# Optimization experiments

Measured on AMD Instinct MI355X. Metric: run time of the kernel, lower is better.

The kernel has to match this reference:

```python
import jax, jax.numpy as jnp
import numpy as np

NUM_HEADS = 32


def setup_inputs() -> dict:
    key = jax.random.key(0)
    ks = jax.random.split(key, 6)
    B, S, D = 1, 2048, 4096
    hd = D // NUM_HEADS  # 128
    x = jax.random.normal(ks[0], (B, S, D), dtype=jnp.float32)
    # true rotary frequencies: freqs_cis = exp(i * t * theta^{-2j/hd})
    inv_freq = 1.0 / (10000.0 ** (jnp.arange(0, hd, 2, dtype=jnp.float32) / hd))  # [hd//2]
    angles = jnp.arange(S, dtype=jnp.float32)[:, None] * inv_freq[None, :]  # [S, hd//2]
    freqs_cos = jnp.cos(angles)
    freqs_sin = jnp.sin(angles)
    scale = 0.02
    wq = jax.random.normal(ks[1], (D, D), dtype=jnp.float32) * scale
    wk = jax.random.normal(ks[2], (D, D), dtype=jnp.float32) * scale
    wv = jax.random.normal(ks[3], (D, D), dtype=jnp.float32) * scale
    wo = jax.random.normal(ks[4], (D, D), dtype=jnp.float32) * scale
    return {"x": x, "freqs_cos": freqs_cos, "freqs_sin": freqs_sin,
            "wq": wq, "wk": wk, "wv": wv, "wo": wo}


def _apply_rope(t, cos, sin):
    # t: [B, S, H, hd]; cos/sin: [S, hd//2]
    B, S, H, hd = t.shape
    tr = t.reshape(B, S, H, hd // 2, 2)
    a, b = tr[..., 0], tr[..., 1]
    c = cos[None, :, None, :]
    s = sin[None, :, None, :]
    out_r = a * c - b * s
    out_i = a * s + b * c
    return jnp.stack([out_r, out_i], axis=-1).reshape(B, S, H, hd)


def reference(x, freqs_cos, freqs_sin, wq, wk, wv, wo):
    B, S, D = x.shape
    H = NUM_HEADS
    hd = D // H
    xq = (x @ wq).reshape(B, S, H, hd)
    xk = (x @ wk).reshape(B, S, H, hd)
    xv = (x @ wv).reshape(B, S, H, hd)
    xq = _apply_rope(xq, freqs_cos, freqs_sin)
    xk = _apply_rope(xk, freqs_cos, freqs_sin)
    # [B, H, S, hd]
    xq = xq.transpose(0, 2, 1, 3)
    xk = xk.transpose(0, 2, 1, 3)
    xv = xv.transpose(0, 2, 1, 3)
    scores = jnp.einsum('bhqd,bhkd->bhqk', xq, xk) / jnp.sqrt(jnp.float32(hd))
    scores = jax.nn.softmax(scores.astype(jnp.float32), axis=-1).astype(xq.dtype)
    out = jnp.einsum('bhqk,bhkd->bhqd', scores, xv)
    out = out.transpose(0, 2, 1, 3).reshape(B, S, D)
    return out @ wo
```

## Files before the change

### kernel.cpp

```cpp
#include <hip/hip_runtime.h>
#include <hip/hip_bf16.h>

typedef __hip_bfloat16 bf16;
typedef __attribute__((ext_vector_type(8))) short short8;
typedef __attribute__((ext_vector_type(4))) short short4v;
typedef __attribute__((ext_vector_type(4))) float f32x4;

#define MFMA16(a, b, c) __builtin_amdgcn_mfma_f32_16x16x32_bf16((a), (b), (c), 0, 0, 0)

static __device__ __forceinline__ void gload_lds16(const bf16* g, bf16* l) {
  __builtin_amdgcn_global_load_lds((const __attribute__((address_space(1))) unsigned int*)g,
                                   (__attribute__((address_space(3))) unsigned int*)l,
                                   16, 0, 0);
}

__global__ __launch_bounds__(256) void castx_kernel(const float* __restrict__ x,
                                                    bf16* __restrict__ xb, int n) {
  int i = (blockIdx.x * 256 + threadIdx.x) * 8;
  if (i >= n) return;
  float4 v0 = *(const float4*)(x + i);
  float4 v1 = *(const float4*)(x + i + 4);
  bf16 tmp[8];
  tmp[0] = __float2bfloat16(v0.x); tmp[1] = __float2bfloat16(v0.y);
  tmp[2] = __float2bfloat16(v0.z); tmp[3] = __float2bfloat16(v0.w);
  tmp[4] = __float2bfloat16(v1.x); tmp[5] = __float2bfloat16(v1.y);
  tmp[6] = __float2bfloat16(v1.z); tmp[7] = __float2bfloat16(v1.w);
  *(short8*)(xb + i) = *(short8*)tmp;
}

__global__ __launch_bounds__(256) void tw_kernel(const float* __restrict__ W,
                                                 bf16* __restrict__ WT) {
  __shared__ bf16 tile[64][65];
  int b = blockIdx.x;
  int tk = (b >> 6) * 64;
  int tn = (b & 63) * 64;
  int t = threadIdx.x;
  int c = t & 63, r0 = t >> 6;
#pragma unroll
  for (int i = 0; i < 16; ++i) {
    int r = i * 4 + r0;
    tile[c][r] = __float2bfloat16(W[(size_t)(tk + r) * 4096 + tn + c]);
  }
  __syncthreads();
#pragma unroll
  for (int i = 0; i < 16; ++i) {
    int r = i * 4 + r0;
    WT[(size_t)(tn + r) * 4096 + tk + c] = tile[r][c];
  }
}

template <int EPI>
__global__ __launch_bounds__(512) void gemm_bt2(const bf16* __restrict__ A,
                                                const bf16* __restrict__ Bt,
                                                void* __restrict__ Cv,
                                                int M, int N, int K,
                                                const float* __restrict__ fcos,
                                                const float* __restrict__ fsin) {
  __shared__ bf16 LDS[3][384 * 64];
  const int NB = N >> 8;
  int bm = blockIdx.x / NB, bn = blockIdx.x % NB;
  int t = threadIdx.x, lane = t & 63, w = t >> 6;
  int wm = w >> 2, wn = w & 3;
  int lr = lane & 15, lg = lane >> 4;
  f32x4 acc[4][4] = {};

  const bf16* Ab = A + (size_t)bm * 128 * K;
  const bf16* Bb = Bt + (size_t)bn * 256 * K;
  int srow = t >> 3;
  int sg = (t & 7) ^ (((t >> 5) & 1) << 1);
  int NK = K >> 6;

#define GSTAGE(buf, kt)                                                         \
  do {                                                                          \
    bf16* l_ = LDS[buf];                                                        \
    const bf16* ga_ = Ab + (size_t)(kt) * 64;                                   \
    _Pragma("unroll") for (int i = 0; i < 2; ++i)                               \
      gload_lds16(ga_ + (size_t)(i * 64 + srow) * K + sg * 8,                   \
                  l_ + (i * 512 + w * 64) * 8);                                 \
    const bf16* gb_ = Bb + (size_t)(kt) * 64;                                   \
    bf16* lb_ = l_ + 128 * 64;                                                  \
    _Pragma("unroll") for (int i = 0; i < 4; ++i)                               \
      gload_lds16(gb_ + (size_t)(i * 64 + srow) * K + sg * 8,                   \
                  lb_ + (i * 512 + w * 64) * 8);                                \
  } while (0)

  GSTAGE(0, 0);
  GSTAGE(1, 1);
  asm volatile("s_waitcnt vmcnt(6)" ::: "memory");
  __builtin_amdgcn_s_barrier();

  int cr = 0;
  for (int kt = 0; kt < NK; ++kt) {
    const bf16* la = LDS[cr];
    const bf16* lb = la + 128 * 64;
    int sw = (lr >> 1) & 2;

    short8 a[4][2], b0[2][2];
#pragma unroll
    for (int m = 0; m < 4; ++m)
#pragma unroll
      for (int kc = 0; kc < 2; ++kc)
        a[m][kc] = *(const short8*)(la + (wm * 64 + m * 16 + lr) * 64 +
                                    (((kc * 4 + lg) ^ sw) << 3));
#pragma unroll
    for (int n2 = 0; n2 < 2; ++n2)
#pragma unroll
      for (int kc = 0; kc < 2; ++kc)
        b0[n2][kc] = *(const short8*)(lb + (wn * 64 + n2 * 16 + lr) * 64 +
                                      (((kc * 4 + lg) ^ sw) << 3));
    int cw = cr + 2; if (cw >= 3) cw -= 3;
    if (kt + 2 < NK) {
      GSTAGE(cw, kt + 2);
      asm volatile("s_waitcnt vmcnt(6)" ::: "memory");
    } else {
      asm volatile("s_waitcnt vmcnt(0)" ::: "memory");
    }
    __builtin_amdgcn_s_barrier();
    __builtin_amdgcn_s_setprio(1);
#pragma unroll
    for (int m = 0; m < 4; ++m)
#pragma unroll
      for (int n2 = 0; n2 < 2; ++n2)
#pragma unroll
        for (int kc = 0; kc < 2; ++kc)
          acc[m][n2] = MFMA16(a[m][kc], b0[n2][kc], acc[m][n2]);
    __builtin_amdgcn_s_setprio(0);
    __builtin_amdgcn_s_barrier();

    short8 b1[2][2];
#pragma unroll
    for (int n2 = 0; n2 < 2; ++n2)
#pragma unroll
      for (int kc = 0; kc < 2; ++kc)
        b1[n2][kc] = *(const short8*)(lb + (wn * 64 + (2 + n2) * 16 + lr) * 64 +
                                      (((kc * 4 + lg) ^ sw) << 3));
    __builtin_amdgcn_s_barrier();
    __builtin_amdgcn_s_setprio(1);
#pragma unroll
    for (int m = 0; m < 4; ++m)
#pragma unroll
      for (int n2 = 0; n2 < 2; ++n2)
#pragma unroll
        for (int kc = 0; kc < 2; ++kc)
          acc[m][2 + n2] = MFMA16(a[m][kc], b1[n2][kc], acc[m][2 + n2]);
    __builtin_amdgcn_s_setprio(0);
    __builtin_amdgcn_s_barrier();

    cr = (cr + 1 == 3) ? 0 : cr + 1;
  }
#undef GSTAGE

#pragma unroll
  for (int m = 0; m < 4; ++m)
#pragma unroll
    for (int nf = 0; nf < 4; ++nf) {
      int col = bn * 256 + wn * 64 + nf * 16 + lr;
      int row0 = bm * 128 + wm * 64 + m * 16 + lg * 4;
      if constexpr (EPI == 1 || EPI == 2) {
        const float qs = (EPI == 1) ? 0.08838834764831845f : 1.0f;
        int ip = (col >> 1) & 63;
        float sgn = (col & 1) ? 1.0f : -1.0f;
#pragma unroll
        for (int r = 0; r < 4; ++r) {
          int row = row0 + r;
          float mine = acc[m][nf][r];
          float oth = __shfl_xor(mine, 1);
          float cv = fcos[row * 64 + ip];
          float sv = fsin[row * 64 + ip];
          float v = (mine * cv + sgn * oth * sv) * qs;
          ((bf16*)Cv)[(size_t)row * N + col] = __float2bfloat16(v);
        }
      } else if constexpr (EPI == 3) {
        bf16 tmp[4];
#pragma unroll
        for (int r = 0; r < 4; ++r) tmp[r] = __float2bfloat16(acc[m][nf][r]);
        *(short4v*)((bf16*)Cv + (size_t)col * M + row0) = *(short4v*)tmp;
      } else {
#pragma unroll
        for (int r = 0; r < 4; ++r) {
          int row = row0 + r;
          if constexpr (EPI == 4)
            ((float*)Cv)[(size_t)row * N + col] = acc[m][nf][r];
          else
            ((bf16*)Cv)[(size_t)row * N + col] = __float2bfloat16(acc[m][nf][r]);
        }
      }
    }
}

__global__ __launch_bounds__(512, 2) void attn_fwd(const bf16* __restrict__ Q,
                                                   const bf16* __restrict__ K,
                                                   const bf16* __restrict__ Vt,
                                                   bf16* __restrict__ O) {
  __shared__ bf16 Kbuf[2][64 * 128];
  __shared__ bf16 Vbuf[2][128 * 64];
  __shared__ char Ps_all[8][2][2048];
  const int S = 2048, D = 4096, HD = 128, NT = 32;
  int g = blockIdx.y * 8 + blockIdx.x;
  int wid = (g & 7) * 32 + (g >> 3);
  int h = wid >> 3, qb = wid & 7;
  int tid = threadIdx.x, lane = tid & 63, w = tid >> 6;
  int lr = lane & 15, lg = lane >> 4;
  int q0 = qb * 256 + w * 32;
  int swz = (lr & 7) << 4;

  const bf16* Kh = K + h * HD;
  const bf16* Vh = Vt + (size_t)h * HD * S;

  short8 aq[2][4];
#pragma unroll
  for (int u = 0; u < 2; ++u)
#pragma unroll
    for (int c = 0; c < 4; ++c)
      aq[u][c] = *(const short8*)(Q + (size_t)(q0 + u * 16 + lr) * D + h * HD + c * 32 + lg * 8);

  int kr = lane >> 4, ksl = lane & 15;
  int vr = lane >> 3, vsl = lane & 7;

  f32x4 accO[2][8] = {};
  float lsum[2] = {0.f, 0.f};

#define STAGE(b, ttile)                                                            \
  do {                                                                             \
    int kv0_ = (ttile) * 64;                                                       \
    _Pragma("unroll") for (int ii = 0; ii < 2; ++ii) {                             \
      int row = w * 8 + ii * 4 + kr;                                               \
      gload_lds16(Kh + (size_t)(kv0_ + row) * D + ((ksl ^ (row & 7)) << 3),        \
                  &Kbuf[b][(w * 8 + ii * 4) * 128]);                               \
    }                                                                              \
    _Pragma("unroll") for (int ii = 0; ii < 2; ++ii) {                             \
      int row = w * 16 + ii * 8 + vr;                                              \
      gload_lds16(Vh + (size_t)row * S + kv0_ + ((vsl ^ (row & 7)) << 3),          \
                  &Vbuf[b][(w * 16 + ii * 8) * 64]);                               \
    }                                                                              \
  } while (0)

  int cur = 0;
  STAGE(0, 0);
  for (int tt = 0; tt < NT; ++tt) {
    if (tt + 1 < NT) {
      STAGE(cur ^ 1, tt + 1);
      asm volatile("s_waitcnt vmcnt(4)" ::: "memory");
    } else {
      asm volatile("s_waitcnt vmcnt(0)" ::: "memory");
    }
    __builtin_amdgcn_s_barrier();
    const bf16* Kb_ = Kbuf[cur];
    const bf16* Vb_ = Vbuf[cur];

    f32x4 sf[2][4] = {};
#pragma unroll
    for (int j = 0; j < 4; ++j)
#pragma unroll
      for (int c = 0; c < 4; ++c) {
        short8 kf = *(const short8*)(Kb_ + (j * 16 + lr) * 128 +
                                     (((c * 4 + lg) ^ (lr & 7)) << 3));
        sf[0][j] = MFMA16(kf, aq[0][c], sf[0][j]);
        sf[1][j] = MFMA16(kf, aq[1][c], sf[1][j]);
      }
#pragma unroll
    for (int u = 0; u < 2; ++u) {
      char* Ps = Ps_all[w][u];
#pragma unroll
      for (int j = 0; j < 4; ++j) {
        float p0 = __expf(sf[u][j][0]);
        float p1 = __expf(sf[u][j][1]);
        float p2 = __expf(sf[u][j][2]);
        float p3 = __expf(sf[u][j][3]);
        lsum[u] += (p0 + p1) + (p2 + p3);
        bf16 pk[4] = {__float2bfloat16(p0), __float2bfloat16(p1),
                      __float2bfloat16(p2), __float2bfloat16(p3)};
        *(short4v*)(Ps + lr * 128 + ((j * 32 + lg * 8) ^ swz)) = *(short4v*)pk;
      }
    }
#pragma unroll
    for (int t2 = 0; t2 < 2; ++t2) {
      short8 pa0 = *(const short8*)(Ps_all[w][0] + lr * 128 + ((t2 * 64 + lg * 16) ^ swz));
      short8 pa1 = *(const short8*)(Ps_all[w][1] + lr * 128 + ((t2 * 64 + lg * 16) ^ swz));
#pragma unroll
      for (int n = 0; n < 8; ++n) {
        short8 bv = *(const short8*)(Vb_ + (n * 16 + lr) * 64 +
                                     (((t2 * 4 + lg) ^ (lr & 7)) << 3));
        accO[0][n] = MFMA16(pa0, bv, accO[0][n]);
        accO[1][n] = MFMA16(pa1, bv, accO[1][n]);
      }
    }
    __builtin_amdgcn_s_barrier();
    cur ^= 1;
  }
#undef STAGE

#pragma unroll
  for (int u = 0; u < 2; ++u) {
    float ls = lsum[u];
    ls += __shfl_xor(ls, 16);
    ls += __shfl_xor(ls, 32);
    float rs[4];
#pragma unroll
    for (int r = 0; r < 4; ++r)
      rs[r] = 1.f / __shfl(ls, lg * 4 + r);
#pragma unroll
    for (int n = 0; n < 8; ++n)
#pragma unroll
      for (int r = 0; r < 4; ++r) {
        int row = q0 + u * 16 + lg * 4 + r;
        int col = h * HD + n * 16 + lr;
        O[(size_t)row * D + col] = __float2bfloat16(accO[u][n][r] * rs[r]);
      }
  }
}

extern "C" void kernel_launch(void* const* d_in, const int* in_sizes, int n_in,
                              void* d_out, int out_size, void* d_ws, size_t ws_size,
                              hipStream_t stream) {
  const float* x    = (const float*)d_in[0];
  const float* fcos = (const float*)d_in[1];
  const float* fsin = (const float*)d_in[2];
  const float* wq   = (const float*)d_in[3];
  const float* wk   = (const float*)d_in[4];
  const float* wv   = (const float*)d_in[5];
  const float* wo   = (const float*)d_in[6];
  float* out = (float*)d_out;

  const int S = 2048, D = 4096;
  const size_t MB = 1024 * 1024;
  char* ws = (char*)d_ws;
  bf16* xb = (bf16*)(ws);
  bf16* wT = (bf16*)(ws + 16 * MB);
  bf16* Qb = (bf16*)(ws + 48 * MB);
  bf16* Kb = (bf16*)(ws + 64 * MB);
  bf16* Vt = (bf16*)(ws + 80 * MB);
  bf16* AO = (bf16*)(ws);

  int n = S * D;
  castx_kernel<<<n / (256 * 8), 256, 0, stream>>>(x, xb, n);

  tw_kernel<<<4096, 256, 0, stream>>>(wq, wT);
  gemm_bt2<1><<<256, 512, 0, stream>>>(xb, wT, Qb, S, D, D, fcos, fsin);
  tw_kernel<<<4096, 256, 0, stream>>>(wk, wT);
  gemm_bt2<2><<<256, 512, 0, stream>>>(xb, wT, Kb, S, D, D, fcos, fsin);
  tw_kernel<<<4096, 256, 0, stream>>>(wv, wT);
  gemm_bt2<3><<<256, 512, 0, stream>>>(xb, wT, Vt, S, D, D, nullptr, nullptr);

  attn_fwd<<<dim3(8, 32), 512, 0, stream>>>(Qb, Kb, Vt, AO);

  tw_kernel<<<4096, 256, 0, stream>>>(wo, wT);
  gemm_bt2<4><<<256, 512, 0, stream>>>(AO, wT, out, S, D, D, nullptr, nullptr);
}
```

Measured before the change: 457.9 us.

## Load A fragments directly into registers and stage only B through LDS

The GEMM is restructured so each wave loads its A operand fragments straight from global memory into registers, and only the B tile goes through LDS with a double buffer and an XOR swizzle. It also adds an XCD-aware block remapping and a launch bound of two blocks per CU. The aim is to cut LDS traffic and footprint and improve L2 locality across chiplets. In exchange, A loads are redundant across the four waves sharing rows, register pressure rises, and the two-stage pipeline is shallower than the previous three-stage one.

```diff
diff --git a/kernel.cpp b/kernel.cpp
--- a/kernel.cpp
+++ b/kernel.cpp
@@ -50,105 +50,120 @@
 }
 
 template <int EPI>
-__global__ __launch_bounds__(512) void gemm_bt2(const bf16* __restrict__ A,
+__global__ __launch_bounds__(512, 2) void gemm3(const bf16* __restrict__ A,
                                                 const bf16* __restrict__ Bt,
                                                 void* __restrict__ Cv,
                                                 int M, int N, int K,
                                                 const float* __restrict__ fcos,
                                                 const float* __restrict__ fsin) {
-  __shared__ bf16 LDS[3][384 * 64];
+  __shared__ bf16 Bs[2][256 * 64];
   const int NB = N >> 8;
-  int bm = blockIdx.x / NB, bn = blockIdx.x % NB;
+  int g = blockIdx.x;
+  int nwg = (M >> 7) * NB;
+  int wid = (g & 7) * (nwg >> 3) + (g >> 3);
+  int bm = wid / NB, bn = wid % NB;
   int t = threadIdx.x, lane = t & 63, w = t >> 6;
   int wm = w >> 2, wn = w & 3;
   int lr = lane & 15, lg = lane >> 4;
   f32x4 acc[4][4] = {};
 
-  const bf16* Ab = A + (size_t)bm * 128 * K;
   const bf16* Bb = Bt + (size_t)bn * 256 * K;
   int srow = t >> 3;
-  int sg = (t & 7) ^ (((t >> 5) & 1) << 1);
+  int sg = (t & 7) ^ (srow & 7);
   int NK = K >> 6;
 
-#define GSTAGE(buf, kt)                                                         \
-  do {                                                                          \
-    bf16* l_ = LDS[buf];                                                        \
-    const bf16* ga_ = Ab + (size_t)(kt) * 64;                                   \
-    _Pragma("unroll") for (int i = 0; i < 2; ++i)                               \
-      gload_lds16(ga_ + (size_t)(i * 64 + srow) * K + sg * 8,                   \
-                  l_ + (i * 512 + w * 64) * 8);                                 \
-    const bf16* gb_ = Bb + (size_t)(kt) * 64;                                   \
-    bf16* lb_ = l_ + 128 * 64;                                                  \
-    _Pragma("unroll") for (int i = 0; i < 4; ++i)                               \
-      gload_lds16(gb_ + (size_t)(i * 64 + srow) * K + sg * 8,                   \
-                  lb_ + (i * 512 + w * 64) * 8);                                \
+  const bf16* arow[4];
+#pragma unroll
+  for (int m = 0; m < 4; ++m)
+    arow[m] = A + (size_t)(bm * 128 + wm * 64 + m * 16 + lr) * K + lg * 8;
+
+#define GSTAGE(buf, kt)                                                    \
+  do {                                                                     \
+    const bf16* gb_ = Bb + (size_t)(kt) * 64;                              \
+    bf16* lb_ = Bs[buf];                                                   \
+    _Pragma("unroll") for (int i = 0; i < 4; ++i)                          \
+      gload_lds16(gb_ + (size_t)(i * 64 + srow) * K + sg * 8,              \
+                  lb_ + (i * 512 + w * 64) * 8);                           \
   } while (0)
 
+#define BFRAG(lb, nf, kc) \
+  (*(const short8*)((lb) + (((wn * 64 + (nf)*16 + lr) * 8 + (((kc)*4 + lg) ^ (lr & 7))) * 8)))
+
+  short8 a0[4][2], a1[4][2];
+#pragma unroll
+  for (int m = 0; m < 4; ++m)
+#pragma unroll
+    for (int kc = 0; kc < 2; ++kc)
+      a0[m][kc] = *(const short8*)(arow[m] + kc * 32);
   GSTAGE(0, 0);
-  GSTAGE(1, 1);
-  asm volatile("s_waitcnt vmcnt(6)" ::: "memory");
-  __builtin_amdgcn_s_barrier();
-
-  int cr = 0;
-  for (int kt = 0; kt < NK; ++kt) {
-    const bf16* la = LDS[cr];
-    const bf16* lb = la + 128 * 64;
-    int sw = (lr >> 1) & 2;
-
-    short8 a[4][2], b0[2][2];
-#pragma unroll
-    for (int m = 0; m < 4; ++m)
-#pragma unroll
-      for (int kc = 0; kc < 2; ++kc)
-        a[m][kc] = *(const short8*)(la + (wm * 64 + m * 16 + lr) * 64 +
-                                    (((kc * 4 + lg) ^ sw) << 3));
-#pragma unroll
-    for (int n2 = 0; n2 < 2; ++n2)
-#pragma unroll
-      for (int kc = 0; kc < 2; ++kc)
-        b0[n2][kc] = *(const short8*)(lb + (wn * 64 + n2 * 16 + lr) * 64 +
-                                      (((kc * 4 + lg) ^ sw) << 3));
-    int cw = cr + 2; if (cw >= 3) cw -= 3;
-    if (kt + 2 < NK) {
-      GSTAGE(cw, kt + 2);
-      asm volatile("s_waitcnt vmcnt(6)" ::: "memory");
+
+  for (int kt = 0; kt < NK; kt += 2) {
+    if (kt + 1 < NK) {
+#pragma unroll
+      for (int m = 0; m < 4; ++m)
+#pragma unroll
+        for (int kc = 0; kc < 2; ++kc)
+          a1[m][kc] = *(const short8*)(arow[m] + (kt + 1) * 64 + kc * 32);
+      GSTAGE(1, kt + 1);
+      asm volatile("s_waitcnt vmcnt(12)" ::: "memory");
     } else {
       asm volatile("s_waitcnt vmcnt(0)" ::: "memory");
     }
     __builtin_amdgcn_s_barrier();
-    __builtin_amdgcn_s_setprio(1);
-#pragma unroll
-    for (int m = 0; m < 4; ++m)
-#pragma unroll
-      for (int n2 = 0; n2 < 2; ++n2)
+    {
+      const bf16* lb = Bs[0];
+      short8 b[4][2];
+#pragma unroll
+      for (int nf = 0; nf < 4; ++nf)
 #pragma unroll
         for (int kc = 0; kc < 2; ++kc)
-          acc[m][n2] = MFMA16(a[m][kc], b0[n2][kc], acc[m][n2]);
-    __builtin_amdgcn_s_setprio(0);
-    __builtin_amdgcn_s_barrier();
-
-    short8 b1[2][2];
-#pragma unroll
-    for (int n2 = 0; n2 < 2; ++n2)
-#pragma unroll
-      for (int kc = 0; kc < 2; ++kc)
-        b1[n2][kc] = *(const short8*)(lb + (wn * 64 + (2 + n2) * 16 + lr) * 64 +
-                                      (((kc * 4 + lg) ^ sw) << 3));
-    __builtin_amdgcn_s_barrier();
-    __builtin_amdgcn_s_setprio(1);
-#pragma unroll
-    for (int m = 0; m < 4; ++m)
-#pragma unroll
-      for (int n2 = 0; n2 < 2; ++n2)
+          b[nf][kc] = BFRAG(lb, nf, kc);
+      __builtin_amdgcn_s_setprio(1);
+#pragma unroll
+      for (int m = 0; m < 4; ++m)
+#pragma unroll
+        for (int nf = 0; nf < 4; ++nf)
+#pragma unroll
+          for (int kc = 0; kc < 2; ++kc)
+            acc[m][nf] = MFMA16(a0[m][kc], b[nf][kc], acc[m][nf]);
+      __builtin_amdgcn_s_setprio(0);
+    }
+    __builtin_amdgcn_s_barrier();
+
+    if (kt + 2 < NK) {
+#pragma unroll
+      for (int m = 0; m < 4; ++m)
 #pragma unroll
         for (int kc = 0; kc < 2; ++kc)
-          acc[m][2 + n2] = MFMA16(a[m][kc], b1[n2][kc], acc[m][2 + n2]);
-    __builtin_amdgcn_s_setprio(0);
-    __builtin_amdgcn_s_barrier();
-
-    cr = (cr + 1 == 3) ? 0 : cr + 1;
+          a0[m][kc] = *(const short8*)(arow[m] + (kt + 2) * 64 + kc * 32);
+      GSTAGE(0, kt + 2);
+      asm volatile("s_waitcnt vmcnt(12)" ::: "memory");
+    } else {
+      asm volatile("s_waitcnt vmcnt(0)" ::: "memory");
+    }
+    __builtin_amdgcn_s_barrier();
+    {
+      const bf16* lb = Bs[1];
+      short8 b[4][2];
+#pragma unroll
+      for (int nf = 0; nf < 4; ++nf)
+#pragma unroll
+        for (int kc = 0; kc < 2; ++kc)
+          b[nf][kc] = BFRAG(lb, nf, kc);
+      __builtin_amdgcn_s_setprio(1);
+#pragma unroll
+      for (int m = 0; m < 4; ++m)
+#pragma unroll
+        for (int nf = 0; nf < 4; ++nf)
+#pragma unroll
+          for (int kc = 0; kc < 2; ++kc)
+            acc[m][nf] = MFMA16(a1[m][kc], b[nf][kc], acc[m][nf]);
+      __builtin_amdgcn_s_setprio(0);
+    }
+    __builtin_amdgcn_s_barrier();
   }
 #undef GSTAGE
+#undef BFRAG
 
 #pragma unroll
   for (int m = 0; m < 4; ++m)
@@ -179,10 +194,7 @@
 #pragma unroll
         for (int r = 0; r < 4; ++r) {
           int row = row0 + r;
-          if constexpr (EPI == 4)
-            ((float*)Cv)[(size_t)row * N + col] = acc[m][nf][r];
-          else
-            ((bf16*)Cv)[(size_t)row * N + col] = __float2bfloat16(acc[m][nf][r]);
+          ((float*)Cv)[(size_t)row * N + col] = acc[m][nf][r];
         }
       }
     }
@@ -336,14 +348,14 @@
   castx_kernel<<<n / (256 * 8), 256, 0, stream>>>(x, xb, n);
 
   tw_kernel<<<4096, 256, 0, stream>>>(wq, wT);
-  gemm_bt2<1><<<256, 512, 0, stream>>>(xb, wT, Qb, S, D, D, fcos, fsin);
+  gemm3<1><<<256, 512, 0, stream>>>(xb, wT, Qb, S, D, D, fcos, fsin);
   tw_kernel<<<4096, 256, 0, stream>>>(wk, wT);
-  gemm_bt2<2><<<256, 512, 0, stream>>>(xb, wT, Kb, S, D, D, fcos, fsin);
+  gemm3<2><<<256, 512, 0, stream>>>(xb, wT, Kb, S, D, D, fcos, fsin);
   tw_kernel<<<4096, 256, 0, stream>>>(wv, wT);
-  gemm_bt2<3><<<256, 512, 0, stream>>>(xb, wT, Vt, S, D, D, nullptr, nullptr);
+  gemm3<3><<<256, 512, 0, stream>>>(xb, wT, Vt, S, D, D, nullptr, nullptr);
 
   attn_fwd<<<dim3(8, 32), 512, 0, stream>>>(Qb, Kb, Vt, AO);
 
   tw_kernel<<<4096, 256, 0, stream>>>(wo, wT);
-  gemm_bt2<4><<<256, 512, 0, stream>>>(AO, wT, out, S, D, D, nullptr, nullptr);
-}
+  gemm3<4><<<256, 512, 0, stream>>>(AO, wT, out, S, D, D, nullptr, nullptr);
+}
```

New measurement: 763.2 us. +66.7%, slower.

## Restructure GEMM main loop into four MFMA quadrants with interleaved prefetch

Applied to the files above, without the earlier changes.

The GEMM inner loop is split into four 2x2 MFMA quadrants, and the next-stage global-to-LDS loads are spread between the quadrants instead of issued in one burst. This aims to overlap memory issue with compute and shrink live register fragments. It also remaps workgroup IDs in an XCD-aware order so neighbouring tiles share L2, and switches the LDS swizzle to a full 8-way row XOR to reduce bank conflicts. The extra barriers add synchronisation overhead, and the generic epilogue now always writes fp32, which only the EPI 4 path uses.

```diff
diff --git a/kernel.cpp b/kernel.cpp
--- a/kernel.cpp
+++ b/kernel.cpp
@@ -50,105 +50,133 @@
 }
 
 template <int EPI>
-__global__ __launch_bounds__(512) void gemm_bt2(const bf16* __restrict__ A,
-                                                const bf16* __restrict__ Bt,
-                                                void* __restrict__ Cv,
-                                                int M, int N, int K,
-                                                const float* __restrict__ fcos,
-                                                const float* __restrict__ fsin) {
+__global__ __launch_bounds__(512) void gemm4(const bf16* __restrict__ A,
+                                             const bf16* __restrict__ Bt,
+                                             void* __restrict__ Cv,
+                                             int M, int N, int K,
+                                             const float* __restrict__ fcos,
+                                             const float* __restrict__ fsin) {
   __shared__ bf16 LDS[3][384 * 64];
   const int NB = N >> 8;
-  int bm = blockIdx.x / NB, bn = blockIdx.x % NB;
+  int g = blockIdx.x;
+  int nwg = (M >> 7) * NB;
+  int wid = (g & 7) * (nwg >> 3) + (g >> 3);
+  int bm = wid / NB, bn = wid % NB;
   int t = threadIdx.x, lane = t & 63, w = t >> 6;
   int wm = w >> 2, wn = w & 3;
   int lr = lane & 15, lg = lane >> 4;
+  int rsw = lr & 7;
   f32x4 acc[4][4] = {};
 
   const bf16* Ab = A + (size_t)bm * 128 * K;
   const bf16* Bb = Bt + (size_t)bn * 256 * K;
   int srow = t >> 3;
-  int sg = (t & 7) ^ (((t >> 5) & 1) << 1);
+  int sg = (t & 7) ^ (srow & 7);
   int NK = K >> 6;
 
-#define GSTAGE(buf, kt)                                                         \
-  do {                                                                          \
-    bf16* l_ = LDS[buf];                                                        \
-    const bf16* ga_ = Ab + (size_t)(kt) * 64;                                   \
-    _Pragma("unroll") for (int i = 0; i < 2; ++i)                               \
-      gload_lds16(ga_ + (size_t)(i * 64 + srow) * K + sg * 8,                   \
-                  l_ + (i * 512 + w * 64) * 8);                                 \
-    const bf16* gb_ = Bb + (size_t)(kt) * 64;                                   \
-    bf16* lb_ = l_ + 128 * 64;                                                  \
-    _Pragma("unroll") for (int i = 0; i < 4; ++i)                               \
-      gload_lds16(gb_ + (size_t)(i * 64 + srow) * K + sg * 8,                   \
-                  lb_ + (i * 512 + w * 64) * 8);                                \
-  } while (0)
-
-  GSTAGE(0, 0);
-  GSTAGE(1, 1);
+#define STA(buf, kt2, i)                                                        \
+  gload_lds16(Ab + (size_t)((i) * 64 + srow) * K + (kt2) * 64 + sg * 8,         \
+              LDS[buf] + ((i) * 512 + w * 64) * 8)
+#define STB(buf, kt2, i)                                                        \
+  gload_lds16(Bb + (size_t)((i) * 64 + srow) * K + (kt2) * 64 + sg * 8,         \
+              LDS[buf] + 128 * 64 + ((i) * 512 + w * 64) * 8)
+#define AFRAG(la, m, kc) \
+  (*(const short8*)((la) + (wm * 64 + (m) * 16 + lr) * 64 + ((((kc) * 4 + lg) ^ rsw) << 3)))
+#define BFRAG(lb, nf, kc) \
+  (*(const short8*)((lb) + (wn * 64 + (nf) * 16 + lr) * 64 + ((((kc) * 4 + lg) ^ rsw) << 3)))
+
+  STA(0, 0, 0); STA(0, 0, 1);
+  STB(0, 0, 0); STB(0, 0, 1); STB(0, 0, 2); STB(0, 0, 3);
+  STA(1, 1, 0); STA(1, 1, 1);
+  STB(1, 1, 0); STB(1, 1, 1); STB(1, 1, 2); STB(1, 1, 3);
   asm volatile("s_waitcnt vmcnt(6)" ::: "memory");
   __builtin_amdgcn_s_barrier();
 
-  int cr = 0;
+  int cur = 0;
   for (int kt = 0; kt < NK; ++kt) {
-    const bf16* la = LDS[cr];
+    const bf16* la = LDS[cur];
     const bf16* lb = la + 128 * 64;
-    int sw = (lr >> 1) & 2;
-
-    short8 a[4][2], b0[2][2];
-#pragma unroll
-    for (int m = 0; m < 4; ++m)
+    int nb2 = cur + 2; if (nb2 >= 3) nb2 -= 3;
+    bool pf = (kt + 2) < NK;
+    short8 a0[2][2], a1[2][2], b0[2][2], b1[2][2];
+
+#pragma unroll
+    for (int i = 0; i < 2; ++i)
+#pragma unroll
+      for (int kc = 0; kc < 2; ++kc) {
+        a0[i][kc] = AFRAG(la, i, kc);
+        b0[i][kc] = BFRAG(lb, i, kc);
+      }
+    if (pf) { STA(nb2, kt + 2, 0); STA(nb2, kt + 2, 1); }
+    __builtin_amdgcn_s_barrier();
+    __builtin_amdgcn_s_setprio(1);
+#pragma unroll
+    for (int i = 0; i < 2; ++i)
+#pragma unroll
+      for (int j = 0; j < 2; ++j)
+#pragma unroll
+        for (int kc = 0; kc < 2; ++kc)
+          acc[i][j] = MFMA16(a0[i][kc], b0[j][kc], acc[i][j]);
+    __builtin_amdgcn_s_setprio(0);
+    __builtin_amdgcn_s_barrier();
+
+#pragma unroll
+    for (int j = 0; j < 2; ++j)
 #pragma unroll
       for (int kc = 0; kc < 2; ++kc)
-        a[m][kc] = *(const short8*)(la + (wm * 64 + m * 16 + lr) * 64 +
-                                    (((kc * 4 + lg) ^ sw) << 3));
-#pragma unroll
-    for (int n2 = 0; n2 < 2; ++n2)
+        b1[j][kc] = BFRAG(lb, 2 + j, kc);
+    if (pf) { STB(nb2, kt + 2, 0); STB(nb2, kt + 2, 1); }
+    __builtin_amdgcn_s_barrier();
+    __builtin_amdgcn_s_setprio(1);
+#pragma unroll
+    for (int i = 0; i < 2; ++i)
+#pragma unroll
+      for (int j = 0; j < 2; ++j)
+#pragma unroll
+        for (int kc = 0; kc < 2; ++kc)
+          acc[i][2 + j] = MFMA16(a0[i][kc], b1[j][kc], acc[i][2 + j]);
+    __builtin_amdgcn_s_setprio(0);
+    __builtin_amdgcn_s_barrier();
+
+#pragma unroll
+    for (int i = 0; i < 2; ++i)
 #pragma unroll
       for (int kc = 0; kc < 2; ++kc)
-        b0[n2][kc] = *(const short8*)(lb + (wn * 64 + n2 * 16 + lr) * 64 +
-                                      (((kc * 4 + lg) ^ sw) << 3));
-    int cw = cr + 2; if (cw >= 3) cw -= 3;
-    if (kt + 2 < NK) {
-      GSTAGE(cw, kt + 2);
+        a1[i][kc] = AFRAG(la, 2 + i, kc);
+    if (pf) { STB(nb2, kt + 2, 2); STB(nb2, kt + 2, 3); }
+    __builtin_amdgcn_s_barrier();
+    __builtin_amdgcn_s_setprio(1);
+#pragma unroll
+    for (int i = 0; i < 2; ++i)
+#pragma unroll
+      for (int j = 0; j < 2; ++j)
+#pragma unroll
+        for (int kc = 0; kc < 2; ++kc)
+          acc[2 + i][j] = MFMA16(a1[i][kc], b0[j][kc], acc[2 + i][j]);
+    __builtin_amdgcn_s_setprio(0);
+    __builtin_amdgcn_s_barrier();
+
+    __builtin_amdgcn_s_setprio(1);
+#pragma unroll
+    for (int i = 0; i < 2; ++i)
+#pragma unroll
+      for (int j = 0; j < 2; ++j)
+#pragma unroll
+        for (int kc = 0; kc < 2; ++kc)
+          acc[2 + i][2 + j] = MFMA16(a1[i][kc], b1[j][kc], acc[2 + i][2 + j]);
+    __builtin_amdgcn_s_setprio(0);
+    if (pf)
       asm volatile("s_waitcnt vmcnt(6)" ::: "memory");
-    } else {
+    else
       asm volatile("s_waitcnt vmcnt(0)" ::: "memory");
-    }
-    __builtin_amdgcn_s_barrier();
-    __builtin_amdgcn_s_setprio(1);
-#pragma unroll
-    for (int m = 0; m < 4; ++m)
-#pragma unroll
-      for (int n2 = 0; n2 < 2; ++n2)
-#pragma unroll
-        for (int kc = 0; kc < 2; ++kc)
-          acc[m][n2] = MFMA16(a[m][kc], b0[n2][kc], acc[m][n2]);
-    __builtin_amdgcn_s_setprio(0);
-    __builtin_amdgcn_s_barrier();
-
-    short8 b1[2][2];
-#pragma unroll
-    for (int n2 = 0; n2 < 2; ++n2)
-#pragma unroll
-      for (int kc = 0; kc < 2; ++kc)
-        b1[n2][kc] = *(const short8*)(lb + (wn * 64 + (2 + n2) * 16 + lr) * 64 +
-                                      (((kc * 4 + lg) ^ sw) << 3));
-    __builtin_amdgcn_s_barrier();
-    __builtin_amdgcn_s_setprio(1);
-#pragma unroll
-    for (int m = 0; m < 4; ++m)
-#pragma unroll
-      for (int n2 = 0; n2 < 2; ++n2)
-#pragma unroll
-        for (int kc = 0; kc < 2; ++kc)
-          acc[m][2 + n2] = MFMA16(a[m][kc], b1[n2][kc], acc[m][2 + n2]);
-    __builtin_amdgcn_s_setprio(0);
-    __builtin_amdgcn_s_barrier();
-
-    cr = (cr + 1 == 3) ? 0 : cr + 1;
-  }
-#undef GSTAGE
+    __builtin_amdgcn_s_barrier();
+
+    cur = (cur + 1 == 3) ? 0 : cur + 1;
+  }
+#undef STA
+#undef STB
+#undef AFRAG
+#undef BFRAG
 
 #pragma unroll
   for (int m = 0; m < 4; ++m)
@@ -179,10 +207,7 @@
 #pragma unroll
         for (int r = 0; r < 4; ++r) {
           int row = row0 + r;
-          if constexpr (EPI == 4)
-            ((float*)Cv)[(size_t)row * N + col] = acc[m][nf][r];
-          else
-            ((bf16*)Cv)[(size_t)row * N + col] = __float2bfloat16(acc[m][nf][r]);
+          ((float*)Cv)[(size_t)row * N + col] = acc[m][nf][r];
         }
       }
     }
@@ -336,14 +361,14 @@
   castx_kernel<<<n / (256 * 8), 256, 0, stream>>>(x, xb, n);
 
   tw_kernel<<<4096, 256, 0, stream>>>(wq, wT);
-  gemm_bt2<1><<<256, 512, 0, stream>>>(xb, wT, Qb, S, D, D, fcos, fsin);
+  gemm4<1><<<256, 512, 0, stream>>>(xb, wT, Qb, S, D, D, fcos, fsin);
   tw_kernel<<<4096, 256, 0, stream>>>(wk, wT);
-  gemm_bt2<2><<<256, 512, 0, stream>>>(xb, wT, Kb, S, D, D, fcos, fsin);
+  gemm4<2><<<256, 512, 0, stream>>>(xb, wT, Kb, S, D, D, fcos, fsin);
   tw_kernel<<<4096, 256, 0, stream>>>(wv, wT);
-  gemm_bt2<3><<<256, 512, 0, stream>>>(xb, wT, Vt, S, D, D, nullptr, nullptr);
+  gemm4<3><<<256, 512, 0, stream>>>(xb, wT, Vt, S, D, D, nullptr, nullptr);
 
   attn_fwd<<<dim3(8, 32), 512, 0, stream>>>(Qb, Kb, Vt, AO);
 
   tw_kernel<<<4096, 256, 0, stream>>>(wo, wT);
-  gemm_bt2<4><<<256, 512, 0, stream>>>(AO, wT, out, S, D, D, nullptr, nullptr);
-}
+  gemm4<4><<<256, 512, 0, stream>>>(AO, wT, out, S, D, D, nullptr, nullptr);
+}
```

Result: no change. 452.1 us (-1.3%).
